# Kernel optimization log

Measured on AMD Instinct MI355X. Metric: run time of the kernel, lower is better.

Reference implementation:

```python
import jax, jax.numpy as jnp
import numpy as np

N_LORAS = 8   # number of adapters (experts)
RANK = 16     # rank per adapter; rmoe = N_LORAS * RANK = 128
TEMP = 1.0    # self.T


def setup_inputs() -> dict:
    key = jax.random.key(0)
    ks = jax.random.split(key, 7)
    B, S, D_IN, D_OUT = 4, 2048, 4096, 4096
    RMOE = N_LORAS * RANK
    x = jax.random.normal(ks[0], (B, S, D_IN), dtype=jnp.float32)
    base_w = jax.random.normal(ks[1], (D_OUT, D_IN), dtype=jnp.float32) / np.sqrt(D_IN)
    base_b = jax.random.normal(ks[2], (D_OUT,), dtype=jnp.float32) * 0.01
    # nn.init.normal_(lora_A.weight, std=1/r); lora_B zero-init in torch, use small random here
    lora_A = jax.random.normal(ks[3], (RMOE, D_IN), dtype=jnp.float32) / RANK
    lora_B = jax.random.normal(ks[4], (D_OUT, RMOE), dtype=jnp.float32) * 0.02
    router_w = jax.random.normal(ks[5], (N_LORAS, D_IN), dtype=jnp.float32) / np.sqrt(D_IN)
    # scaling[name] = lora_alpha / sqrt(r) per adapter (use_rslora)
    scalings = jnp.full((N_LORAS,), 32.0 / np.sqrt(RANK), dtype=jnp.float32)
    return {"x": x, "base_w": base_w, "base_b": base_b, "lora_A": lora_A,
            "lora_B": lora_B, "router_w": router_w, "scalings": scalings, "top_k": 2}


def reference(x, base_w, base_b, lora_A, lora_B, router_w, scalings, top_k):
    # Base dense layer: y = x W^T + b
    base_out = jnp.einsum('bsd,od->bso', x, base_w) + base_b

    # Router: per-token logits over adapters, top-k, softmax over selected
    logits = jnp.einsum('bsd,ed->bse', x, router_w) / TEMP          # [B,S,E]
    topv, topi = jax.lax.top_k(logits, top_k)                        # [B,S,K]
    gate_k = jax.nn.softmax(topv, axis=-1)                           # [B,S,K]
    # dense per-expert gate: scatter top-k weights back to E slots
    gate_e = jnp.sum(jax.nn.one_hot(topi, N_LORAS, dtype=gate_k.dtype)
                     * gate_k[..., None], axis=-2)                   # [B,S,E]

    # Fused LoRA: h = x A^T over the concatenated rank dim, mask ranks by gate*scaling
    h = jnp.einsum('bsd,rd->bsr', x, lora_A)                         # [B,S,RMOE]
    rank_w = jnp.repeat(gate_e * scalings, RANK, axis=-1)            # [B,S,RMOE]
    lora_out = jnp.einsum('bsr,or->bso', h * rank_w, lora_B)         # [B,S,O]

    return base_out + lora_out
```

## Files before the change

### kernel.cpp

```cpp
#include <hip/hip_runtime.h>
#include <cstdint>

typedef unsigned short u16;
typedef float  f32x4 __attribute__((ext_vector_type(4)));
typedef short  s16x4 __attribute__((ext_vector_type(4)));
typedef short  s16x8 __attribute__((ext_vector_type(8)));

#define D_IN  4096
#define D_OUT 4096
#define RMOE  128
#define KAUG  4224
#define NTOK  8192

__device__ __forceinline__ u16 f2bf(float f) {
    unsigned u = __builtin_bit_cast(unsigned, f);
    unsigned r = u + 0x7fffu + ((u >> 16) & 1u);
    return (u16)(r >> 16);
}

__device__ __forceinline__ void gload16(const void* g, void* l) {
    __builtin_amdgcn_global_load_lds(
        (const __attribute__((address_space(1))) void*)g,
        (__attribute__((address_space(3))) void*)l, 16, 0, 0);
}

__global__ __launch_bounds__(256)
void prep_kernel(const float* __restrict__ x, const float* __restrict__ rw,
                 const float* __restrict__ scal, const float* __restrict__ bw,
                 const float* __restrict__ lA, const float* __restrict__ lB,
                 u16* __restrict__ Xaug, u16* __restrict__ Waug,
                 u16* __restrict__ A16, float* __restrict__ gates) {
    if (blockIdx.x < 2048) {
        int wave = threadIdx.x >> 6, lane = threadIdx.x & 63;
        int t = blockIdx.x * 4 + wave;
        const float4* xp = (const float4*)(x + (long)t * D_IN);
        u16* xa = Xaug + (long)t * KAUG;
        float acc[8];
#pragma unroll
        for (int e = 0; e < 8; ++e) acc[e] = 0.f;
#pragma unroll 4
        for (int i = 0; i < 16; ++i) {
            float4 xv = xp[i * 64 + lane];
            s16x4 o;
            o[0] = (short)f2bf(xv.x); o[1] = (short)f2bf(xv.y);
            o[2] = (short)f2bf(xv.z); o[3] = (short)f2bf(xv.w);
            *(s16x4*)(xa + (i * 64 + lane) * 4) = o;
#pragma unroll
            for (int e = 0; e < 8; ++e) {
                float4 wv = ((const float4*)(rw + (long)e * D_IN))[i * 64 + lane];
                acc[e] += xv.x * wv.x + xv.y * wv.y + xv.z * wv.z + xv.w * wv.w;
            }
        }
#pragma unroll
        for (int e = 0; e < 8; ++e) {
#pragma unroll
            for (int off = 32; off > 0; off >>= 1)
                acc[e] += __shfl_xor(acc[e], off, 64);
        }
        if (lane == 0) {
            int i1 = 0; float v1 = acc[0];
#pragma unroll
            for (int e = 1; e < 8; ++e) if (acc[e] > v1) { v1 = acc[e]; i1 = e; }
            int i2 = -1; float v2 = -3.4e38f;
#pragma unroll
            for (int e = 0; e < 8; ++e) if (e != i1 && acc[e] > v2) { v2 = acc[e]; i2 = e; }
            float g1 = 1.f / (1.f + expf(v2 - v1));
            float g2 = 1.f - g1;
            float* gp = gates + (long)t * 8;
#pragma unroll
            for (int e = 0; e < 8; ++e)
                gp[e] = (e == i1) ? g1 * scal[e] : ((e == i2) ? g2 * scal[e] : 0.f);
        }
    } else {
        const long nw = (long)D_OUT * D_IN / 8;
        const long nb = (long)D_OUT * RMOE / 8;
        long tid = (long)(blockIdx.x - 2048) * 256 + threadIdx.x;
        const float* src; u16* dst;
        if (tid < nw) {
            long e = tid * 8; long row = e >> 12; long col = e & 4095;
            src = bw + e; dst = Waug + row * KAUG + col;
        } else if (tid < nw + nb) {
            long e = (tid - nw) * 8; long row = e >> 7; long col = e & 127;
            src = lB + e; dst = Waug + row * KAUG + D_IN + col;
        } else {
            long e = (tid - nw - nb) * 8;
            src = lA + e; dst = A16 + e;
        }
        float4 a = ((const float4*)src)[0];
        float4 b = ((const float4*)src)[1];
        s16x8 o;
        o[0] = (short)f2bf(a.x); o[1] = (short)f2bf(a.y);
        o[2] = (short)f2bf(a.z); o[3] = (short)f2bf(a.w);
        o[4] = (short)f2bf(b.x); o[5] = (short)f2bf(b.y);
        o[6] = (short)f2bf(b.z); o[7] = (short)f2bf(b.w);
        *(s16x8*)dst = o;
    }
}

__global__ __launch_bounds__(256)
void lora_h_kernel(u16* __restrict__ Xaug, const u16* __restrict__ A16,
                   const float* __restrict__ gates) {
    __shared__ u16 sX[64 * 32];
    __shared__ u16 sW[32 * 32];
    int tid = threadIdx.x, wave = tid >> 6, lane = tid & 63;
    int bm = blockIdx.x >> 2, bn = blockIdx.x & 3;
    long m0 = (long)bm * 64; int n0 = bn * 32;
    int wr = wave >> 1, wc = wave & 1;
    int rowA = tid >> 2, oct = tid & 3;
    const u16* gx = Xaug + (m0 + rowA) * KAUG + oct * 8;
    const u16* gw = A16 + (long)(n0 + rowA) * D_IN + oct * 8;
    u16* lx = sX + wave * 512;
    u16* lw = sW + wave * 512;
    int cl = lane & 15, kh = lane >> 4;
    int aoff[2];
#pragma unroll
    for (int i = 0; i < 2; ++i)
        aoff[i] = (wr * 32 + i * 16 + cl) * 32 + kh * 8;
    int boff = (wc * 16 + cl) * 32 + kh * 8;
    f32x4 acc2[2];
    acc2[0] = (f32x4){0.f, 0.f, 0.f, 0.f};
    acc2[1] = (f32x4){0.f, 0.f, 0.f, 0.f};
    for (int kt = 0; kt < 128; ++kt) {
        __syncthreads();
        gload16(gx, lx);
        if (tid < 128) gload16(gw, lw);
        gx += 32; gw += 32;
        __syncthreads();
        s16x8 a[2], b;
        a[0] = *(const s16x8*)&sX[aoff[0]];
        a[1] = *(const s16x8*)&sX[aoff[1]];
        b = *(const s16x8*)&sW[boff];
#pragma unroll
        for (int mi = 0; mi < 2; ++mi)
            acc2[mi] = __builtin_amdgcn_mfma_f32_16x16x32_bf16(
                a[mi], b, acc2[mi], 0, 0, 0);
    }
    int col = n0 + wc * 16 + cl;
    int g = col >> 4;
#pragma unroll
    for (int mi = 0; mi < 2; ++mi) {
#pragma unroll
        for (int r = 0; r < 4; ++r) {
            long tok = m0 + wr * 32 + mi * 16 + kh * 4 + r;
            float v = acc2[mi][r] * gates[tok * 8 + g];
            Xaug[tok * KAUG + D_IN + col] = f2bf(v);
        }
    }
}

__global__ __launch_bounds__(512, 2)
void main_gemm(const u16* __restrict__ Xaug, const u16* __restrict__ Waug,
               const float* __restrict__ bias, float* __restrict__ out) {
    __shared__ u16 lds[4 * 16384];
    const int tid = threadIdx.x;
    const int wave = tid >> 6, lane = tid & 63;
    const int cl = lane & 15, kh = lane >> 4;
    const int wr = wave >> 2, wc = wave & 3;

    int bid = blockIdx.x;
    int swz = (bid & 7) * 64 + (bid >> 3);
    long m0 = (long)(swz & 31) * 256;
    long n0 = (long)(swz >> 5) * 256;

    const int rA = tid >> 2;
    const int sl = (((tid & 3) ^ ((tid >> 3) & 3))) * 8;
    const u16* gA0 = Xaug + (m0 + rA) * KAUG + sl;
    const u16* gA1 = Xaug + (m0 + 128 + rA) * KAUG + sl;
    const u16* gB0 = Waug + (n0 + rA) * KAUG + sl;
    const u16* gB1 = Waug + (n0 + 128 + rA) * KAUG + sl;
    const int wbase = wave * 512;

    const int swk = (kh ^ ((cl >> 1) & 3)) * 8;
    const int aob = (wr * 128 + cl) * 32 + swk;
    const int bob = 8192 + (wc * 64 + cl) * 32 + swk;

    f32x4 acc[8][4];
#pragma unroll
    for (int m = 0; m < 8; ++m)
#pragma unroll
        for (int n = 0; n < 4; ++n) acc[m][n] = (f32x4){0.f, 0.f, 0.f, 0.f};

#define STAGE(t) do { u16* L = lds + ((t) & 3) * 16384 + wbase;              \
        gload16(gA0 + (t) * 32, L);                                          \
        gload16(gA1 + (t) * 32, L + 4096);                                   \
        gload16(gB0 + (t) * 32, L + 8192);                                   \
        gload16(gB1 + (t) * 32, L + 12288); } while (0)
#define READL(av, bv, Lb) do {                                               \
        _Pragma("unroll")                                                    \
        for (int m_ = 0; m_ < 8; ++m_)                                       \
            av[m_] = *(const s16x8*)&(Lb)[aob + m_ * 512];                   \
        _Pragma("unroll")                                                    \
        for (int n_ = 0; n_ < 4; ++n_)                                       \
            bv[n_] = *(const s16x8*)&(Lb)[bob + n_ * 512]; } while (0)
#define DOMFMA(av, bv) do {                                                  \
        __builtin_amdgcn_s_setprio(1);                                       \
        _Pragma("unroll")                                                    \
        for (int m_ = 0; m_ < 8; ++m_)                                       \
            _Pragma("unroll")                                                \
            for (int n_ = 0; n_ < 4; ++n_)                                   \
                acc[m_][n_] = __builtin_amdgcn_mfma_f32_16x16x32_bf16(       \
                    av[m_], bv[n_], acc[m_][n_], 0, 0, 0);                   \
        __builtin_amdgcn_s_setprio(0); } while (0)

    s16x8 av0[8], bv0[4], av1[8], bv1[4];

    STAGE(0); STAGE(1); STAGE(2);
    asm volatile("s_waitcnt vmcnt(8)" ::: "memory");
    __builtin_amdgcn_s_barrier();
    __builtin_amdgcn_sched_barrier(0);
    READL(av0, bv0, (lds + 0));

    for (int u = 0; u < 66; ++u) {
        const int tA = 2 * u, tB = 2 * u + 1;
        if (tA <= 128) asm volatile("s_waitcnt vmcnt(4)" ::: "memory");
        else           asm volatile("s_waitcnt vmcnt(0)" ::: "memory");
        __builtin_amdgcn_s_barrier();
        __builtin_amdgcn_sched_barrier(0);
        {
            const u16* Lb = lds + (tB & 3) * 16384;
            READL(av1, bv1, Lb);
            if (tA + 3 < 132) STAGE(tA + 3);
        }
        asm volatile("s_waitcnt lgkmcnt(12)" ::: "memory");
        __builtin_amdgcn_sched_barrier(0);
        DOMFMA(av0, bv0);
        if (tB < 131) {
            asm volatile("s_waitcnt vmcnt(4)" ::: "memory");
            __builtin_amdgcn_s_barrier();
            __builtin_amdgcn_sched_barrier(0);
            {
                const u16* Lb = lds + ((tB + 1) & 3) * 16384;
                READL(av0, bv0, Lb);
                if (tB + 3 < 132) STAGE(tB + 3);
            }
            asm volatile("s_waitcnt lgkmcnt(12)" ::: "memory");
            __builtin_amdgcn_sched_barrier(0);
        } else {
            asm volatile("s_waitcnt lgkmcnt(0)" ::: "memory");
            __builtin_amdgcn_sched_barrier(0);
        }
        DOMFMA(av1, bv1);
    }
#undef STAGE
#undef READL
#undef DOMFMA

#pragma unroll
    for (int n = 0; n < 4; ++n) {
        long col = n0 + wc * 64 + n * 16 + cl;
        float bvv = bias[col];
#pragma unroll
        for (int m = 0; m < 8; ++m) {
            long row = m0 + wr * 128 + m * 16 + kh * 4;
#pragma unroll
            for (int r = 0; r < 4; ++r)
                out[(row + r) * (long)D_OUT + col] = acc[m][n][r] + bvv;
        }
    }
}

extern "C" void kernel_launch(void* const* d_in, const int* in_sizes, int n_in,
                              void* d_out, int out_size, void* d_ws, size_t ws_size,
                              hipStream_t stream) {
    const float* x  = (const float*)d_in[0];
    const float* bw = (const float*)d_in[1];
    const float* bb = (const float*)d_in[2];
    const float* lA = (const float*)d_in[3];
    const float* lB = (const float*)d_in[4];
    const float* rw = (const float*)d_in[5];
    const float* sc = (const float*)d_in[6];
    float* out = (float*)d_out;

    char* ws = (char*)d_ws;
    u16* Xaug  = (u16*)ws;
    u16* Waug  = (u16*)(ws + 69206016);
    u16* A16   = (u16*)(ws + 103809024);
    float* gates = (float*)(ws + 104857600);

    prep_kernel<<<10752, 256, 0, stream>>>(x, rw, sc, bw, lA, lB,
                                           Xaug, Waug, A16, gates);
    lora_h_kernel<<<512, 256, 0, stream>>>(Xaug, A16, gates);
    main_gemm<<<512, 512, 0, stream>>>(Xaug, Waug, bb, out);
}
```

Before: 388.3 us.

## Shrink main GEMM tile to 256x128 with simple double buffering and higher occupancy

Cuts the main GEMM block tile from 256x256 to 256x128, doubling the grid to 1024 blocks and the per-wave accumulator footprint in half. The 4-stage LDS ring with interleaved dual register sets is replaced by a plain 2-stage double buffer that waits for all loads each step. Launch bounds now request 4 blocks per CU, trading data reuse per tile and deep prefetch for more occupancy and lower register pressure. This raises global/L2 traffic per FLOP and exposes more load latency per iteration.

```diff
diff --git a/kernel.cpp b/kernel.cpp
--- a/kernel.cpp
+++ b/kernel.cpp
@@ -148,110 +148,76 @@
     }
 }
 
-__global__ __launch_bounds__(512, 2)
+__global__ __launch_bounds__(512, 4)
 void main_gemm(const u16* __restrict__ Xaug, const u16* __restrict__ Waug,
                const float* __restrict__ bias, float* __restrict__ out) {
-    __shared__ u16 lds[4 * 16384];
+    __shared__ u16 lds[2 * 12288];
     const int tid = threadIdx.x;
     const int wave = tid >> 6, lane = tid & 63;
     const int cl = lane & 15, kh = lane >> 4;
-    const int wr = wave >> 2, wc = wave & 3;
+    const int wr = wave >> 1, wc = wave & 1;
 
     int bid = blockIdx.x;
-    int swz = (bid & 7) * 64 + (bid >> 3);
+    int swz = (bid & 7) * 128 + (bid >> 3);
     long m0 = (long)(swz & 31) * 256;
-    long n0 = (long)(swz >> 5) * 256;
+    long n0 = (long)(swz >> 5) * 128;
 
     const int rA = tid >> 2;
     const int sl = (((tid & 3) ^ ((tid >> 3) & 3))) * 8;
     const u16* gA0 = Xaug + (m0 + rA) * KAUG + sl;
     const u16* gA1 = Xaug + (m0 + 128 + rA) * KAUG + sl;
     const u16* gB0 = Waug + (n0 + rA) * KAUG + sl;
-    const u16* gB1 = Waug + (n0 + 128 + rA) * KAUG + sl;
     const int wbase = wave * 512;
 
     const int swk = (kh ^ ((cl >> 1) & 3)) * 8;
-    const int aob = (wr * 128 + cl) * 32 + swk;
+    const int aob = (wr * 64 + cl) * 32 + swk;
     const int bob = 8192 + (wc * 64 + cl) * 32 + swk;
 
-    f32x4 acc[8][4];
-#pragma unroll
-    for (int m = 0; m < 8; ++m)
+    f32x4 acc[4][4];
+#pragma unroll
+    for (int m = 0; m < 4; ++m)
 #pragma unroll
         for (int n = 0; n < 4; ++n) acc[m][n] = (f32x4){0.f, 0.f, 0.f, 0.f};
 
-#define STAGE(t) do { u16* L = lds + ((t) & 3) * 16384 + wbase;              \
+#define STAGE(t) do { u16* L = lds + ((t) & 1) * 12288 + wbase;              \
         gload16(gA0 + (t) * 32, L);                                          \
         gload16(gA1 + (t) * 32, L + 4096);                                   \
-        gload16(gB0 + (t) * 32, L + 8192);                                   \
-        gload16(gB1 + (t) * 32, L + 12288); } while (0)
-#define READL(av, bv, Lb) do {                                               \
-        _Pragma("unroll")                                                    \
-        for (int m_ = 0; m_ < 8; ++m_)                                       \
-            av[m_] = *(const s16x8*)&(Lb)[aob + m_ * 512];                   \
-        _Pragma("unroll")                                                    \
-        for (int n_ = 0; n_ < 4; ++n_)                                       \
-            bv[n_] = *(const s16x8*)&(Lb)[bob + n_ * 512]; } while (0)
-#define DOMFMA(av, bv) do {                                                  \
-        __builtin_amdgcn_s_setprio(1);                                       \
-        _Pragma("unroll")                                                    \
-        for (int m_ = 0; m_ < 8; ++m_)                                       \
-            _Pragma("unroll")                                                \
-            for (int n_ = 0; n_ < 4; ++n_)                                   \
-                acc[m_][n_] = __builtin_amdgcn_mfma_f32_16x16x32_bf16(       \
-                    av[m_], bv[n_], acc[m_][n_], 0, 0, 0);                   \
-        __builtin_amdgcn_s_setprio(0); } while (0)
-
-    s16x8 av0[8], bv0[4], av1[8], bv1[4];
-
-    STAGE(0); STAGE(1); STAGE(2);
-    asm volatile("s_waitcnt vmcnt(8)" ::: "memory");
-    __builtin_amdgcn_s_barrier();
-    __builtin_amdgcn_sched_barrier(0);
-    READL(av0, bv0, (lds + 0));
-
-    for (int u = 0; u < 66; ++u) {
-        const int tA = 2 * u, tB = 2 * u + 1;
-        if (tA <= 128) asm volatile("s_waitcnt vmcnt(4)" ::: "memory");
-        else           asm volatile("s_waitcnt vmcnt(0)" ::: "memory");
+        gload16(gB0 + (t) * 32, L + 8192); } while (0)
+
+    s16x8 av[4], bv[4];
+
+    STAGE(0);
+
+    for (int t = 0; t < 132; ++t) {
+        asm volatile("s_waitcnt vmcnt(0)" ::: "memory");
         __builtin_amdgcn_s_barrier();
         __builtin_amdgcn_sched_barrier(0);
-        {
-            const u16* Lb = lds + (tB & 3) * 16384;
-            READL(av1, bv1, Lb);
-            if (tA + 3 < 132) STAGE(tA + 3);
-        }
-        asm volatile("s_waitcnt lgkmcnt(12)" ::: "memory");
+        if (t + 1 < 132) STAGE(t + 1);
+        const u16* Lb = lds + (t & 1) * 12288;
+#pragma unroll
+        for (int m = 0; m < 4; ++m) av[m] = *(const s16x8*)&Lb[aob + m * 512];
+#pragma unroll
+        for (int n = 0; n < 4; ++n) bv[n] = *(const s16x8*)&Lb[bob + n * 512];
+        asm volatile("s_waitcnt lgkmcnt(0)" ::: "memory");
         __builtin_amdgcn_sched_barrier(0);
-        DOMFMA(av0, bv0);
-        if (tB < 131) {
-            asm volatile("s_waitcnt vmcnt(4)" ::: "memory");
-            __builtin_amdgcn_s_barrier();
-            __builtin_amdgcn_sched_barrier(0);
-            {
-                const u16* Lb = lds + ((tB + 1) & 3) * 16384;
-                READL(av0, bv0, Lb);
-                if (tB + 3 < 132) STAGE(tB + 3);
-            }
-            asm volatile("s_waitcnt lgkmcnt(12)" ::: "memory");
-            __builtin_amdgcn_sched_barrier(0);
-        } else {
-            asm volatile("s_waitcnt lgkmcnt(0)" ::: "memory");
-            __builtin_amdgcn_sched_barrier(0);
-        }
-        DOMFMA(av1, bv1);
+        __builtin_amdgcn_s_setprio(1);
+#pragma unroll
+        for (int m = 0; m < 4; ++m)
+#pragma unroll
+            for (int n = 0; n < 4; ++n)
+                acc[m][n] = __builtin_amdgcn_mfma_f32_16x16x32_bf16(
+                    av[m], bv[n], acc[m][n], 0, 0, 0);
+        __builtin_amdgcn_s_setprio(0);
     }
 #undef STAGE
-#undef READL
-#undef DOMFMA
 
 #pragma unroll
     for (int n = 0; n < 4; ++n) {
         long col = n0 + wc * 64 + n * 16 + cl;
         float bvv = bias[col];
 #pragma unroll
-        for (int m = 0; m < 8; ++m) {
-            long row = m0 + wr * 128 + m * 16 + kh * 4;
+        for (int m = 0; m < 4; ++m) {
+            long row = m0 + wr * 64 + m * 16 + kh * 4;
 #pragma unroll
             for (int r = 0; r < 4; ++r)
                 out[(row + r) * (long)D_OUT + col] = acc[m][n][r] + bvv;
@@ -280,5 +246,5 @@
     prep_kernel<<<10752, 256, 0, stream>>>(x, rw, sc, bw, lA, lB,
                                            Xaug, Waug, A16, gates);
     lora_h_kernel<<<512, 256, 0, stream>>>(Xaug, A16, gates);
-    main_gemm<<<512, 512, 0, stream>>>(Xaug, Waug, bb, out);
-}
+    main_gemm<<<1024, 512, 0, stream>>>(Xaug, Waug, bb, out);
+}
```

Result: slower. 418.4 us (+7.8%).
